# Kernel optimization log

Hardware: AMD Instinct MI355X
Metric: run time of the kernel (lower is better)

## Reference

```python
import jax, jax.numpy as jnp
import numpy as np

P = 8          # patch_size
HEADS = 4      # patch_size // 2
DIM = 256      # nf*P*P // 16
DH = DIM // HEADS


def setup_inputs() -> dict:
    key = jax.random.key(0)
    ks = jax.random.split(key, 8)
    B, N, C, H, W = 8, 1, 64, 256, 256
    Np = (H // P) * (W // P)           # 1024
    patch_dim = C * P * P              # 4096
    s = 0.02
    return {
        "x": jax.random.normal(ks[0], (B, N, C, H, W), jnp.float32),
        "W_embed": jax.random.normal(ks[1], (DIM, patch_dim), jnp.float32) * s,
        "b_embed": jnp.zeros((DIM,), jnp.float32),
        "pos": jax.random.normal(ks[2], (1, Np, DIM), jnp.float32),
        "Wq": jax.random.normal(ks[3], (DIM, DIM), jnp.float32) * s,
        "Wk": jax.random.normal(ks[4], (Np, Np), jnp.float32) * s,
        "Wv": jax.random.normal(ks[5], (DIM, DIM), jnp.float32) * s,
        "Wout": jax.random.normal(ks[6], (patch_dim, DIM), jnp.float32) * s,
        "b_out": jnp.zeros((patch_dim,), jnp.float32),
    }


def reference(x, W_embed, b_embed, pos, Wq, Wk, Wv, Wout, b_out):
    B, N, C, H, W = x.shape
    Hp, Wp = H // P, W // P
    Np = Hp * Wp
    patch_dim = C * P * P
    BN = B * N

    # unfold (non-overlapping patches), column order = (C, kh, kw)
    xb = x.reshape(BN, C, Hp, P, Wp, P)
    patches = xb.transpose(0, 2, 4, 1, 3, 5).reshape(BN, Np, patch_dim)

    # linear_embed + positional embedding
    emb = jnp.einsum('bnp,dp->bnd', patches, W_embed) + b_embed + pos  # (BN, Np, DIM)

    # q: linear, split heads, mean over head-dim (AvgPool1d(dh) on length dh)
    q = jnp.einsum('bnd,ed->bne', emb, Wq)
    q = q.reshape(BN, Np, HEADS, DH).transpose(0, 2, 1, 3)  # (BN, H, Np, DH)
    q = q.mean(axis=-1)                                      # (BN, H, Np)

    # k = sigmoid(linear_k(q)); diag_embed(k) @ v == k[..., None] * v
    k = jax.nn.sigmoid(jnp.einsum('bhn,mn->bhm', q, Wk))     # (BN, H, Np)

    v = jnp.einsum('bnd,ed->bne', emb, Wv)
    v = v.reshape(BN, Np, HEADS, DH).transpose(0, 2, 1, 3)   # (BN, H, Np, DH)

    out = k[..., None] * v                                   # (BN, H, Np, DH)
    out = out.transpose(0, 2, 1, 3).reshape(BN, Np, DIM)

    out = jnp.einsum('bnd,pd->bnp', out, Wout) + b_out       # (BN, Np, patch_dim)

    # fold back to image
    out = out.reshape(BN, Hp, Wp, C, P, P).transpose(0, 3, 1, 4, 2, 5)
    out = out.reshape(B, N, C, H, W)
    return out
```

## Files before the change

### kernel.cpp

```cpp
#include <hip/hip_runtime.h>

typedef __attribute__((ext_vector_type(8))) short short8;
typedef __attribute__((ext_vector_type(4))) float f32x4;

#define LDA 72
#define KST 260

__device__ __forceinline__ unsigned short f2bf(float f) {
  unsigned int u = __builtin_bit_cast(unsigned int, f);
  u += 0x7fffu + ((u >> 16) & 1u);
  return (unsigned short)(u >> 16);
}
__device__ __forceinline__ float bf2f(unsigned short us) {
  return __builtin_bit_cast(float, (unsigned int)us << 16);
}

__device__ __forceinline__ short8 cvt8(float4 lo, float4 hi) {
  short8 v;
  v[0] = (short)f2bf(lo.x); v[1] = (short)f2bf(lo.y);
  v[2] = (short)f2bf(lo.z); v[3] = (short)f2bf(lo.w);
  v[4] = (short)f2bf(hi.x); v[5] = (short)f2bf(hi.y);
  v[6] = (short)f2bf(hi.z); v[7] = (short)f2bf(hi.w);
  return v;
}

__device__ __forceinline__ void mfma_tile(const unsigned short* __restrict__ Ab,
                                          const unsigned short* __restrict__ Bb,
                                          int wm, int wn, int lr, int lq,
                                          f32x4 (&acc)[2][4]) {
#pragma unroll
  for (int kc = 0; kc < 2; ++kc) {
    short8 a0 = *(const short8*)&Ab[(wm * 32 + lr) * LDA + kc * 32 + lq * 8];
    short8 a1 = *(const short8*)&Ab[(wm * 32 + 16 + lr) * LDA + kc * 32 + lq * 8];
#pragma unroll
    for (int ni = 0; ni < 4; ++ni) {
      short8 b = *(const short8*)&Bb[(wn * 64 + ni * 16 + lr) * LDA + kc * 32 + lq * 8];
      acc[0][ni] = __builtin_amdgcn_mfma_f32_16x16x32_bf16(a0, b, acc[0][ni], 0, 0, 0);
      acc[1][ni] = __builtin_amdgcn_mfma_f32_16x16x32_bf16(a1, b, acc[1][ni], 0, 0, 0);
    }
  }
}

__device__ __forceinline__ void cvt_block(const float* __restrict__ src,
                                          unsigned short* __restrict__ dst, int b) {
  int i = b * 256 + threadIdx.x;
  float4 f = ((const float4*)src)[i];
  unsigned int lo = (unsigned int)f2bf(f.x) | ((unsigned int)f2bf(f.y) << 16);
  unsigned int hi = (unsigned int)f2bf(f.z) | ((unsigned int)f2bf(f.w) << 16);
  uint2 u; u.x = lo; u.y = hi;
  ((uint2*)dst)[i] = u;
}

__global__ __launch_bounds__(256) void prep_kernel(
    const float* __restrict__ W_embed, const float* __restrict__ Wout,
    const float* __restrict__ Wv, const float* __restrict__ Wq,
    unsigned short* __restrict__ Wb, unsigned short* __restrict__ Wob,
    unsigned short* __restrict__ Wvb, float* __restrict__ WqR) {
  int b = blockIdx.x;
  if (b < 1024) { cvt_block(W_embed, Wb, b); return; }
  if (b < 2048) { cvt_block(Wout, Wob, b - 1024); return; }
  if (b < 2112) { cvt_block(Wv, Wvb, b - 2048); return; }
  int idx = (b - 2112) * 256 + threadIdx.x;
  int h = idx >> 8, e = idx & 255;
  float s = 0.f;
  for (int j = 0; j < 64; ++j) s += Wq[(size_t)(h * 64 + j) * 256 + e];
  WqR[idx] = s * (1.f / 64.f);
}

struct StageG1 { float4 a0, a1, a2, a3; short8 b0, b1; };

__device__ __forceinline__ void g1_load(StageG1& s, const float* q0, const float* q1,
                                        const unsigned short* b0, const unsigned short* b1) {
  s.a0 = *(const float4*)q0; s.a1 = *(const float4*)(q0 + 4);
  s.a2 = *(const float4*)q1; s.a3 = *(const float4*)(q1 + 4);
  s.b0 = *(const short8*)b0; s.b1 = *(const short8*)b1;
}

__device__ __forceinline__ void g1_write(unsigned short* Aw, unsigned short* Bw,
                                         int dA0, int dA1, int dB0, int dB1,
                                         const StageG1& s) {
  *(short8*)&Aw[dA0] = cvt8(s.a0, s.a1);
  *(short8*)&Aw[dA1] = cvt8(s.a2, s.a3);
  *(short8*)&Bw[dB0] = s.b0;
  *(short8*)&Bw[dB1] = s.b1;
}

__global__ __launch_bounds__(512, 4) void gemm1_embed(
    const float* __restrict__ x, const unsigned short* __restrict__ Wb,
    float* __restrict__ part) {
  __shared__ __align__(16) unsigned short sm[2][2][128 * LDA];
  const int nt = blockIdx.x, mt = blockIdx.y, sk = blockIdx.z;
  const int m0 = mt * 128, n0 = nt * 128;
  const int t = threadIdx.x;
  const int wave = t >> 6, lane = t & 63;
  const int wm = wave >> 1, wn = wave & 1;
  const int lr = lane & 15, lq = lane >> 4;

  const int bn = m0 >> 10;
  const int ph0 = (m0 & 1023) >> 5;

  const int uA0 = t >> 5, colA = t & 31;
  const int uA1 = uA0 + 16;
  const float* xA = x + ((size_t)(bn << 6) << 16);
  const float* pa0 = xA + (size_t)(((ph0 + (uA0 >> 3)) << 3) + (uA0 & 7)) * 256 + (colA << 3);
  const float* pa1 = xA + (size_t)(((ph0 + (uA1 >> 3)) << 3) + (uA1 & 7)) * 256 + (colA << 3);
  const int dA0 = (((uA0 >> 3) << 5) + colA) * LDA + ((uA0 & 7) << 3);
  const int dA1 = (((uA1 >> 3) << 5) + colA) * LDA + ((uA1 & 7) << 3);

  const int nB0 = t >> 3, kB = t & 7;
  const int nB1 = nB0 + 64;
  const unsigned short* pb0 = Wb + (size_t)(n0 + nB0) * 4096 + (kB << 3);
  const unsigned short* pb1 = Wb + (size_t)(n0 + nB1) * 4096 + (kB << 3);
  const int dB0 = nB0 * LDA + (kB << 3);
  const int dB1 = nB1 * LDA + (kB << 3);

  f32x4 acc[2][4];
#pragma unroll
  for (int i = 0; i < 2; i++)
#pragma unroll
    for (int j = 0; j < 4; j++) acc[i][j] = f32x4{0.f, 0.f, 0.f, 0.f};

  unsigned short* A0 = &sm[0][0][0]; unsigned short* B0 = &sm[0][1][0];
  unsigned short* A1 = &sm[1][0][0]; unsigned short* B1 = &sm[1][1][0];

  StageG1 st0, st1;
  const int kt0 = sk * 16;
  g1_load(st0, pa0 + (size_t)kt0 * 65536, pa1 + (size_t)kt0 * 65536,
          pb0 + (size_t)kt0 * 64, pb1 + (size_t)kt0 * 64);
  g1_load(st1, pa0 + (size_t)(kt0 + 1) * 65536, pa1 + (size_t)(kt0 + 1) * 65536,
          pb0 + (size_t)(kt0 + 1) * 64, pb1 + (size_t)(kt0 + 1) * 64);
  g1_write(A0, B0, dA0, dA1, dB0, dB1, st0);
  __syncthreads();

#pragma unroll 1
  for (int p = 0; p < 7; ++p) {
    const int kb = kt0 + 2 * p;
    g1_load(st0, pa0 + (size_t)(kb + 2) * 65536, pa1 + (size_t)(kb + 2) * 65536,
            pb0 + (size_t)(kb + 2) * 64, pb1 + (size_t)(kb + 2) * 64);
    mfma_tile(A0, B0, wm, wn, lr, lq, acc);
    g1_write(A1, B1, dA0, dA1, dB0, dB1, st1);
    __syncthreads();
    g1_load(st1, pa0 + (size_t)(kb + 3) * 65536, pa1 + (size_t)(kb + 3) * 65536,
            pb0 + (size_t)(kb + 3) * 64, pb1 + (size_t)(kb + 3) * 64);
    mfma_tile(A1, B1, wm, wn, lr, lq, acc);
    g1_write(A0, B0, dA0, dA1, dB0, dB1, st0);
    __syncthreads();
  }
  mfma_tile(A0, B0, wm, wn, lr, lq, acc);
  g1_write(A1, B1, dA0, dA1, dB0, dB1, st1);
  __syncthreads();
  mfma_tile(A1, B1, wm, wn, lr, lq, acc);

  float* pdst = part + (size_t)sk * 2097152;
#pragma unroll
  for (int mi = 0; mi < 2; ++mi)
#pragma unroll
    for (int ni = 0; ni < 4; ++ni) {
      int col = n0 + wn * 64 + ni * 16 + lr;
      int rbase = m0 + wm * 32 + mi * 16 + lq * 4;
#pragma unroll
      for (int r2 = 0; r2 < 4; ++r2)
        pdst[(size_t)(rbase + r2) * 256 + col] = acc[mi][ni][r2];
    }
}

__global__ __launch_bounds__(256) void finq_kernel(
    const float* __restrict__ part, const float* __restrict__ b_embed,
    const float* __restrict__ pos, const float* __restrict__ WqR,
    unsigned short* __restrict__ emb_bf, float* __restrict__ q) {
  __shared__ float wq[1024];
  const int t = threadIdx.x;
  for (int i = t; i < 1024; i += 256) wq[i] = WqR[i];
  __syncthreads();
  const int row_l = t >> 3, seg = t & 7;
  const int row = blockIdx.x * 32 + row_l;
  const int bn = row >> 10, n = row & 1023;
  const float4* p4 = (const float4*)part;
  const float4* b4 = (const float4*)b_embed;
  const float4* pos4 = (const float4*)pos;
  const float4* wq4 = (const float4*)wq;
  const int idx0 = row * 64 + seg * 8;

  float4 e[8];
#pragma unroll
  for (int j = 0; j < 8; ++j) {
    float4 v = p4[idx0 + j];
    float4 v1 = p4[524288 + idx0 + j];
    float4 v2 = p4[1048576 + idx0 + j];
    float4 v3 = p4[1572864 + idx0 + j];
    float4 bb = b4[seg * 8 + j];
    float4 pp = pos4[(size_t)n * 64 + seg * 8 + j];
    e[j].x = v.x + v1.x + v2.x + v3.x + bb.x + pp.x;
    e[j].y = v.y + v1.y + v2.y + v3.y + bb.y + pp.y;
    e[j].z = v.z + v1.z + v2.z + v3.z + bb.z + pp.z;
    e[j].w = v.w + v1.w + v2.w + v3.w + bb.w + pp.w;
  }
  unsigned int ub[16];
#pragma unroll
  for (int j = 0; j < 8; ++j) {
    ub[2 * j]     = (unsigned int)f2bf(e[j].x) | ((unsigned int)f2bf(e[j].y) << 16);
    ub[2 * j + 1] = (unsigned int)f2bf(e[j].z) | ((unsigned int)f2bf(e[j].w) << 16);
  }
  uint4* dst = (uint4*)(emb_bf + (size_t)row * 256 + seg * 32);
#pragma unroll
  for (int j = 0; j < 4; ++j)
    dst[j] = make_uint4(ub[4 * j], ub[4 * j + 1], ub[4 * j + 2], ub[4 * j + 3]);
  float s[4] = {0.f, 0.f, 0.f, 0.f};
#pragma unroll
  for (int h = 0; h < 4; ++h)
#pragma unroll
    for (int j = 0; j < 8; ++j) {
      float4 w = wq4[h * 64 + seg * 8 + j];
      s[h] += e[j].x * w.x + e[j].y * w.y + e[j].z * w.z + e[j].w * w.w;
    }
#pragma unroll
  for (int h = 0; h < 4; ++h) {
    s[h] += __shfl_xor(s[h], 1);
    s[h] += __shfl_xor(s[h], 2);
    s[h] += __shfl_xor(s[h], 4);
  }
  if (seg == 0) {
#pragma unroll
    for (int h = 0; h < 4; ++h)
      q[(size_t)(bn * 4 + h) * 1024 + n] = s[h];
  }
}

__global__ __launch_bounds__(256) void k_kernel(const float* __restrict__ q,
                                                const float* __restrict__ Wk,
                                                float* __restrict__ kk) {
  __shared__ float wk_s[8 * KST];
  __shared__ float q_s[32 * KST];
  const int m0 = blockIdx.x * 8;
  const int t = threadIdx.x;
  const int m = t & 7, bh = t >> 3;
  const float4* wkg = (const float4*)Wk;
  const float4* qg = (const float4*)q;
  float acc = 0.f;
  for (int kt = 0; kt < 4; ++kt) {
    const int k0 = kt * 256;
#pragma unroll
    for (int i = 0; i < 2; ++i) {
      int idx = t + i * 256;
      int r = idx >> 6, c4 = idx & 63;
      *(float4*)&wk_s[r * KST + c4 * 4] = wkg[((size_t)(m0 + r) * 1024 + k0) / 4 + c4];
    }
#pragma unroll
    for (int i = 0; i < 8; ++i) {
      int idx = t + i * 256;
      int r = idx >> 6, c4 = idx & 63;
      *(float4*)&q_s[r * KST + c4 * 4] = qg[((size_t)r * 1024 + k0) / 4 + c4];
    }
    __syncthreads();
#pragma unroll 8
    for (int k4 = 0; k4 < 64; ++k4) {
      float4 a = *(const float4*)&wk_s[m * KST + k4 * 4];
      float4 b = *(const float4*)&q_s[bh * KST + k4 * 4];
      acc += a.x * b.x + a.y * b.y + a.z * b.z + a.w * b.w;
    }
    __syncthreads();
  }
  kk[(size_t)bh * 1024 + m0 + m] = 1.f / (1.f + __expf(-acc));
}

#define VST 264
__global__ __launch_bounds__(256) void vgemm_kernel(
    const unsigned short* __restrict__ Abf, const unsigned short* __restrict__ Wvb,
    const float* __restrict__ kk, unsigned short* __restrict__ ov) {
  __shared__ __align__(16) unsigned short Vs[128 * VST];
  const int nt = blockIdx.x, mt = blockIdx.y;
  const int m0 = mt * 64, n0 = nt * 64;
  const int t = threadIdx.x;
  const int wave = t >> 6, lane = t & 63;
  const int wr = wave >> 1, wc = wave & 1;
  const int lr = lane & 15, lq = lane >> 4;

  const int row0 = t >> 5, kb = t & 31;
#pragma unroll
  for (int i = 0; i < 8; ++i)
    *(short8*)&Vs[(row0 + i * 8) * VST + kb * 8] =
        *(const short8*)(Abf + (size_t)(m0 + row0 + i * 8) * 256 + kb * 8);
#pragma unroll
  for (int i = 0; i < 8; ++i)
    *(short8*)&Vs[(64 + row0 + i * 8) * VST + kb * 8] =
        *(const short8*)(Wvb + (size_t)(n0 + row0 + i * 8) * 256 + kb * 8);
  __syncthreads();

  f32x4 acc[2][2];
#pragma unroll
  for (int i = 0; i < 2; ++i)
#pragma unroll
    for (int j = 0; j < 2; ++j) acc[i][j] = f32x4{0.f, 0.f, 0.f, 0.f};

#pragma unroll
  for (int kc = 0; kc < 8; ++kc) {
    short8 a0 = *(const short8*)&Vs[(wr * 32 + lr) * VST + kc * 32 + lq * 8];
    short8 a1 = *(const short8*)&Vs[(wr * 32 + 16 + lr) * VST + kc * 32 + lq * 8];
    short8 b0 = *(const short8*)&Vs[(64 + wc * 32 + lr) * VST + kc * 32 + lq * 8];
    short8 b1 = *(const short8*)&Vs[(64 + wc * 32 + 16 + lr) * VST + kc * 32 + lq * 8];
    acc[0][0] = __builtin_amdgcn_mfma_f32_16x16x32_bf16(a0, b0, acc[0][0], 0, 0, 0);
    acc[0][1] = __builtin_amdgcn_mfma_f32_16x16x32_bf16(a0, b1, acc[0][1], 0, 0, 0);
    acc[1][0] = __builtin_amdgcn_mfma_f32_16x16x32_bf16(a1, b0, acc[1][0], 0, 0, 0);
    acc[1][1] = __builtin_amdgcn_mfma_f32_16x16x32_bf16(a1, b1, acc[1][1], 0, 0, 0);
  }

#pragma unroll
  for (int mi = 0; mi < 2; ++mi)
#pragma unroll
    for (int ni = 0; ni < 2; ++ni) {
      int col = n0 + wc * 32 + ni * 16 + lr;
      int h = col >> 6;
      int rbase = m0 + wr * 32 + mi * 16 + lq * 4;
#pragma unroll
      for (int r2 = 0; r2 < 4; ++r2) {
        int row = rbase + r2;
        int bn = row >> 10, n = row & 1023;
        float g = kk[(size_t)(bn * 4 + h) * 1024 + n];
        ov[(size_t)row * 256 + col] = f2bf(acc[mi][ni][r2] * g);
      }
    }
}

#define CST 132
struct StageG2 { short8 a[2]; short8 b[4]; };

__device__ __forceinline__ void g2_load(StageG2& s, const unsigned short* pA,
                                        const unsigned short* pB, int k0) {
#pragma unroll
  for (int i = 0; i < 2; ++i)
    s.a[i] = *(const short8*)(pA + (size_t)i * 32 * 256 + k0);
#pragma unroll
  for (int i = 0; i < 4; ++i)
    s.b[i] = *(const short8*)(pB + (size_t)i * 32 * 256 + k0);
}
__device__ __forceinline__ void g2_write(unsigned short* Ab, unsigned short* Bb,
                                         int dA, int dB, const StageG2& s) {
#pragma unroll
  for (int i = 0; i < 2; ++i) *(short8*)&Ab[dA + i * 32 * LDA] = s.a[i];
#pragma unroll
  for (int i = 0; i < 4; ++i) *(short8*)&Bb[dB + i * 32 * LDA] = s.b[i];
}

__global__ __launch_bounds__(256, 2) void gemm2_out(
    const unsigned short* __restrict__ Abf, const unsigned short* __restrict__ Wob,
    const float* __restrict__ b_out, float* __restrict__ out) {
  __shared__ __align__(16) unsigned short smbuf[2][192 * LDA];
  float* csm = (float*)&smbuf[0][0];
  const int nt = blockIdx.x, mt = blockIdx.y;
  const int m0 = mt * 64, n0 = nt * 128;
  const int t = threadIdx.x;
  const int wave = t >> 6, lane = t & 63;
  const int wm = wave >> 1, wn = wave & 1;
  const int lr = lane & 15, lq = lane >> 4;

  unsigned short* A0 = &smbuf[0][0]; unsigned short* B0 = &smbuf[0][64 * LDA];
  unsigned short* A1 = &smbuf[1][0]; unsigned short* B1 = &smbuf[1][64 * LDA];

  const unsigned short* pA = Abf + (size_t)(m0 + (t >> 3)) * 256 + (t & 7) * 8;
  const unsigned short* pB = Wob + (size_t)(n0 + (t >> 3)) * 256 + (t & 7) * 8;
  const int dA = (t >> 3) * LDA + (t & 7) * 8;
  const int dB = dA;

  f32x4 acc[2][4];
#pragma unroll
  for (int i = 0; i < 2; i++)
#pragma unroll
    for (int j = 0; j < 4; j++) acc[i][j] = f32x4{0.f, 0.f, 0.f, 0.f};

  StageG2 st0, st1;
  g2_load(st0, pA, pB, 0);
  g2_load(st1, pA, pB, 64);
  g2_write(A0, B0, dA, dB, st0);
  __syncthreads();
  g2_load(st0, pA, pB, 128);
  mfma_tile(A0, B0, wm, wn, lr, lq, acc);
  g2_write(A1, B1, dA, dB, st1);
  __syncthreads();
  g2_load(st1, pA, pB, 192);
  mfma_tile(A1, B1, wm, wn, lr, lq, acc);
  g2_write(A0, B0, dA, dB, st0);
  __syncthreads();
  mfma_tile(A0, B0, wm, wn, lr, lq, acc);
  g2_write(A1, B1, dA, dB, st1);
  __syncthreads();
  mfma_tile(A1, B1, wm, wn, lr, lq, acc);
  __syncthreads();

#pragma unroll
  for (int mi = 0; mi < 2; ++mi)
#pragma unroll
    for (int ni = 0; ni < 4; ++ni) {
      int pl = wn * 64 + ni * 16 + lr;
      int mb = wm * 32 + mi * 16 + lq * 4;
#pragma unroll
      for (int r2 = 0; r2 < 4; ++r2)
        csm[(mb + r2) * CST + pl] = acc[mi][ni][r2];
    }
  __syncthreads();
  const int bn = m0 >> 10;
  const int ph0 = (m0 & 1023) >> 5;
  const int c0 = n0 >> 6;
#pragma unroll
  for (int i = 0; i < 8; ++i) {
    int idx4 = t + i * 256;
    int kw4 = idx4 & 1;
    int pw = (idx4 >> 1) & 31;
    int kh = (idx4 >> 6) & 7;
    int c2 = (idx4 >> 9) & 1;
    int ph = (idx4 >> 10) & 1;
    int m_local = ph * 32 + pw;
    int p_local = c2 * 64 + kh * 8 + kw4 * 4;
    float4 v = *(const float4*)&csm[m_local * CST + p_local];
    float4 bo = *(const float4*)(b_out + n0 + p_local);
    v.x += bo.x; v.y += bo.y; v.z += bo.z; v.w += bo.w;
    size_t addr = ((size_t)((bn << 6) + c0 + c2) << 16) +
                  (size_t)(((ph0 + ph) << 3) + kh) * 256 + (pw << 3) + kw4 * 4;
    *(float4*)(out + addr) = v;
  }
}

extern "C" void kernel_launch(void* const* d_in, const int* in_sizes, int n_in,
                              void* d_out, int out_size, void* d_ws, size_t ws_size,
                              hipStream_t stream) {
  const float* x       = (const float*)d_in[0];
  const float* W_embed = (const float*)d_in[1];
  const float* b_embed = (const float*)d_in[2];
  const float* pos     = (const float*)d_in[3];
  const float* Wq      = (const float*)d_in[4];
  const float* Wk      = (const float*)d_in[5];
  const float* Wv      = (const float*)d_in[6];
  const float* Wout    = (const float*)d_in[7];
  const float* b_out   = (const float*)d_in[8];
  float* out = (float*)d_out;

  char* ws = (char*)d_ws;
  const size_t MB = 1024 * 1024;
  float* part            = (float*)(ws);
  unsigned short* ov     = (unsigned short*)(ws);
  unsigned short* emb_bf = (unsigned short*)(ws + 32 * MB);
  unsigned short* Wb     = (unsigned short*)(ws + 36 * MB);
  unsigned short* Wob    = (unsigned short*)(ws + 38 * MB);
  unsigned short* Wvb    = (unsigned short*)(ws + 40 * MB);
  float* q               = (float*)(ws + 40 * MB + 131072);
  float* kk              = (float*)(ws + 40 * MB + 262144);
  float* WqR             = (float*)(ws + 40 * MB + 393216);

  prep_kernel<<<2116, 256, 0, stream>>>(W_embed, Wout, Wv, Wq, Wb, Wob, Wvb, WqR);
  gemm1_embed<<<dim3(2, 64, 4), 512, 0, stream>>>(x, Wb, part);
  finq_kernel<<<256, 256, 0, stream>>>(part, b_embed, pos, WqR, emb_bf, q);
  k_kernel<<<128, 256, 0, stream>>>(q, Wk, kk);
  vgemm_kernel<<<dim3(4, 128), 256, 0, stream>>>(emb_bf, Wvb, kk, ov);
  gemm2_out<<<dim3(32, 128), 256, 0, stream>>>(ov, Wob, b_out, out);
}
```

Baseline: 334.0 us.

## Fuse embed GEMM with bias/pos/q epilogue, drop split-K partials

Replaces the split-K embed GEMM (128x128 tiles, 4 K-splits writing fp32 partials) and the separate finalize kernel with one kernel. Each block computes a 32x256 output tile over the full K and applies bias, positional embedding, bf16 conversion and the q projection from LDS. This removes the 32MB partial-sum round trip and one launch. In exchange the grid shrinks to 256 blocks of 256 threads with a long serial K loop, and each block rereads the full W_embed slice, which may lower parallelism and raise weight traffic.

```diff
diff --git a/kernel.cpp b/kernel.cpp
--- a/kernel.cpp
+++ b/kernel.cpp
@@ -67,52 +67,38 @@
   WqR[idx] = s * (1.f / 64.f);
 }
 
-struct StageG1 { float4 a0, a1, a2, a3; short8 b0, b1; };
-
-__device__ __forceinline__ void g1_load(StageG1& s, const float* q0, const float* q1,
-                                        const unsigned short* b0, const unsigned short* b1) {
-  s.a0 = *(const float4*)q0; s.a1 = *(const float4*)(q0 + 4);
-  s.a2 = *(const float4*)q1; s.a3 = *(const float4*)(q1 + 4);
-  s.b0 = *(const short8*)b0; s.b1 = *(const short8*)b1;
-}
-
-__device__ __forceinline__ void g1_write(unsigned short* Aw, unsigned short* Bw,
-                                         int dA0, int dA1, int dB0, int dB1,
-                                         const StageG1& s) {
-  *(short8*)&Aw[dA0] = cvt8(s.a0, s.a1);
-  *(short8*)&Aw[dA1] = cvt8(s.a2, s.a3);
-  *(short8*)&Bw[dB0] = s.b0;
-  *(short8*)&Bw[dB1] = s.b1;
-}
-
-__global__ __launch_bounds__(512, 4) void gemm1_embed(
+struct StageV3 { float4 a0, a1; short8 b[8]; };
+
+__global__ __launch_bounds__(256, 1) void gemm1_fused(
     const float* __restrict__ x, const unsigned short* __restrict__ Wb,
-    float* __restrict__ part) {
-  __shared__ __align__(16) unsigned short sm[2][2][128 * LDA];
-  const int nt = blockIdx.x, mt = blockIdx.y, sk = blockIdx.z;
-  const int m0 = mt * 128, n0 = nt * 128;
+    const float* __restrict__ b_embed, const float* __restrict__ pos,
+    const float* __restrict__ WqR,
+    unsigned short* __restrict__ emb_bf, float* __restrict__ q) {
+  __shared__ __align__(16) unsigned short lds[41472];
+  __shared__ float wq_s[1024];
+  unsigned short* A0 = lds;
+  unsigned short* A1 = lds + 2304;
+  unsigned short* B0 = lds + 4608;
+  unsigned short* B1 = lds + 23040;
+  float* esm = (float*)(lds + 4608);
+
   const int t = threadIdx.x;
   const int wave = t >> 6, lane = t & 63;
-  const int wm = wave >> 1, wn = wave & 1;
+  const int wn = wave;
   const int lr = lane & 15, lq = lane >> 4;
-
+  const int m0 = blockIdx.x * 32;
   const int bn = m0 >> 10;
-  const int ph0 = (m0 & 1023) >> 5;
-
-  const int uA0 = t >> 5, colA = t & 31;
-  const int uA1 = uA0 + 16;
-  const float* xA = x + ((size_t)(bn << 6) << 16);
-  const float* pa0 = xA + (size_t)(((ph0 + (uA0 >> 3)) << 3) + (uA0 & 7)) * 256 + (colA << 3);
-  const float* pa1 = xA + (size_t)(((ph0 + (uA1 >> 3)) << 3) + (uA1 & 7)) * 256 + (colA << 3);
-  const int dA0 = (((uA0 >> 3) << 5) + colA) * LDA + ((uA0 & 7) << 3);
-  const int dA1 = (((uA1 >> 3) << 5) + colA) * LDA + ((uA1 & 7) << 3);
-
-  const int nB0 = t >> 3, kB = t & 7;
-  const int nB1 = nB0 + 64;
-  const unsigned short* pb0 = Wb + (size_t)(n0 + nB0) * 4096 + (kB << 3);
-  const unsigned short* pb1 = Wb + (size_t)(n0 + nB1) * 4096 + (kB << 3);
-  const int dB0 = nB0 * LDA + (kB << 3);
-  const int dB1 = nB1 * LDA + (kB << 3);
+  const int nbase = m0 & 1023;
+  const int ph = nbase >> 5;
+
+  for (int i = t; i < 1024; i += 256) wq_s[i] = WqR[i];
+
+  const int mA = t >> 3, kc8 = t & 7;
+  const float* pa = x + ((size_t)(bn << 6) << 16) +
+                    (size_t)((ph << 3) + kc8) * 256 + (mA << 3);
+  const int dA = mA * LDA + (kc8 << 3);
+  const unsigned short* pb = Wb + (size_t)(t >> 3) * 4096 + ((t & 7) << 3);
+  const int dB = (t >> 3) * LDA + ((t & 7) << 3);
 
   f32x4 acc[2][4];
 #pragma unroll
@@ -120,110 +106,105 @@
 #pragma unroll
     for (int j = 0; j < 4; j++) acc[i][j] = f32x4{0.f, 0.f, 0.f, 0.f};
 
-  unsigned short* A0 = &sm[0][0][0]; unsigned short* B0 = &sm[0][1][0];
-  unsigned short* A1 = &sm[1][0][0]; unsigned short* B1 = &sm[1][1][0];
-
-  StageG1 st0, st1;
-  const int kt0 = sk * 16;
-  g1_load(st0, pa0 + (size_t)kt0 * 65536, pa1 + (size_t)kt0 * 65536,
-          pb0 + (size_t)kt0 * 64, pb1 + (size_t)kt0 * 64);
-  g1_load(st1, pa0 + (size_t)(kt0 + 1) * 65536, pa1 + (size_t)(kt0 + 1) * 65536,
-          pb0 + (size_t)(kt0 + 1) * 64, pb1 + (size_t)(kt0 + 1) * 64);
-  g1_write(A0, B0, dA0, dA1, dB0, dB1, st0);
+  StageV3 st0, st1;
+#define G1F_LOAD(st, kt)                                                         \
+  {                                                                              \
+    const float* qa = pa + (size_t)(kt) * 65536;                                 \
+    st.a0 = *(const float4*)qa; st.a1 = *(const float4*)(qa + 4);                \
+    _Pragma("unroll")                                                            \
+    for (int i = 0; i < 8; ++i)                                                  \
+      st.b[i] = *(const short8*)(pb + (size_t)i * 131072 + (kt) * 64);           \
+  }
+#define G1F_WRITE(st, Aw, Bw)                                                    \
+  {                                                                              \
+    *(short8*)&Aw[dA] = cvt8(st.a0, st.a1);                                      \
+    _Pragma("unroll")                                                            \
+    for (int i = 0; i < 8; ++i) *(short8*)&Bw[dB + i * 32 * LDA] = st.b[i];      \
+  }
+
+  G1F_LOAD(st0, 0)
+  G1F_LOAD(st1, 1)
+  G1F_WRITE(st0, A0, B0)
   __syncthreads();
 
 #pragma unroll 1
-  for (int p = 0; p < 7; ++p) {
-    const int kb = kt0 + 2 * p;
-    g1_load(st0, pa0 + (size_t)(kb + 2) * 65536, pa1 + (size_t)(kb + 2) * 65536,
-            pb0 + (size_t)(kb + 2) * 64, pb1 + (size_t)(kb + 2) * 64);
-    mfma_tile(A0, B0, wm, wn, lr, lq, acc);
-    g1_write(A1, B1, dA0, dA1, dB0, dB1, st1);
+  for (int p = 0; p < 31; ++p) {
+    G1F_LOAD(st0, 2 * p + 2)
+    mfma_tile(A0, B0, 0, wn, lr, lq, acc);
+    G1F_WRITE(st1, A1, B1)
     __syncthreads();
-    g1_load(st1, pa0 + (size_t)(kb + 3) * 65536, pa1 + (size_t)(kb + 3) * 65536,
-            pb0 + (size_t)(kb + 3) * 64, pb1 + (size_t)(kb + 3) * 64);
-    mfma_tile(A1, B1, wm, wn, lr, lq, acc);
-    g1_write(A0, B0, dA0, dA1, dB0, dB1, st0);
+    G1F_LOAD(st1, 2 * p + 3)
+    mfma_tile(A1, B1, 0, wn, lr, lq, acc);
+    G1F_WRITE(st0, A0, B0)
     __syncthreads();
   }
-  mfma_tile(A0, B0, wm, wn, lr, lq, acc);
-  g1_write(A1, B1, dA0, dA1, dB0, dB1, st1);
-  __syncthreads();
-  mfma_tile(A1, B1, wm, wn, lr, lq, acc);
-
-  float* pdst = part + (size_t)sk * 2097152;
+  mfma_tile(A0, B0, 0, wn, lr, lq, acc);
+  G1F_WRITE(st1, A1, B1)
+  __syncthreads();
+  mfma_tile(A1, B1, 0, wn, lr, lq, acc);
+
 #pragma unroll
   for (int mi = 0; mi < 2; ++mi)
 #pragma unroll
     for (int ni = 0; ni < 4; ++ni) {
-      int col = n0 + wn * 64 + ni * 16 + lr;
-      int rbase = m0 + wm * 32 + mi * 16 + lq * 4;
+      int col = wn * 64 + ni * 16 + lr;
+      int rb = mi * 16 + lq * 4;
 #pragma unroll
       for (int r2 = 0; r2 < 4; ++r2)
-        pdst[(size_t)(rbase + r2) * 256 + col] = acc[mi][ni][r2];
-    }
-}
-
-__global__ __launch_bounds__(256) void finq_kernel(
-    const float* __restrict__ part, const float* __restrict__ b_embed,
-    const float* __restrict__ pos, const float* __restrict__ WqR,
-    unsigned short* __restrict__ emb_bf, float* __restrict__ q) {
-  __shared__ float wq[1024];
-  const int t = threadIdx.x;
-  for (int i = t; i < 1024; i += 256) wq[i] = WqR[i];
-  __syncthreads();
-  const int row_l = t >> 3, seg = t & 7;
-  const int row = blockIdx.x * 32 + row_l;
-  const int bn = row >> 10, n = row & 1023;
-  const float4* p4 = (const float4*)part;
-  const float4* b4 = (const float4*)b_embed;
-  const float4* pos4 = (const float4*)pos;
-  const float4* wq4 = (const float4*)wq;
-  const int idx0 = row * 64 + seg * 8;
-
-  float4 e[8];
-#pragma unroll
-  for (int j = 0; j < 8; ++j) {
-    float4 v = p4[idx0 + j];
-    float4 v1 = p4[524288 + idx0 + j];
-    float4 v2 = p4[1048576 + idx0 + j];
-    float4 v3 = p4[1572864 + idx0 + j];
-    float4 bb = b4[seg * 8 + j];
-    float4 pp = pos4[(size_t)n * 64 + seg * 8 + j];
-    e[j].x = v.x + v1.x + v2.x + v3.x + bb.x + pp.x;
-    e[j].y = v.y + v1.y + v2.y + v3.y + bb.y + pp.y;
-    e[j].z = v.z + v1.z + v2.z + v3.z + bb.z + pp.z;
-    e[j].w = v.w + v1.w + v2.w + v3.w + bb.w + pp.w;
-  }
-  unsigned int ub[16];
-#pragma unroll
-  for (int j = 0; j < 8; ++j) {
-    ub[2 * j]     = (unsigned int)f2bf(e[j].x) | ((unsigned int)f2bf(e[j].y) << 16);
-    ub[2 * j + 1] = (unsigned int)f2bf(e[j].z) | ((unsigned int)f2bf(e[j].w) << 16);
-  }
-  uint4* dst = (uint4*)(emb_bf + (size_t)row * 256 + seg * 32);
-#pragma unroll
-  for (int j = 0; j < 4; ++j)
-    dst[j] = make_uint4(ub[4 * j], ub[4 * j + 1], ub[4 * j + 2], ub[4 * j + 3]);
-  float s[4] = {0.f, 0.f, 0.f, 0.f};
-#pragma unroll
-  for (int h = 0; h < 4; ++h)
+        esm[(rb + r2) * 264 + col] = acc[mi][ni][r2];
+    }
+  __syncthreads();
+
+  {
+    const int row = t >> 3, seg = t & 7;
+    const int n = nbase + row;
+    const float4* e4 = (const float4*)esm;
+    const float4* b4 = (const float4*)b_embed;
+    const float4* pos4 = (const float4*)pos;
+    const float4* wq4 = (const float4*)wq_s;
+    float4 e[8];
 #pragma unroll
     for (int j = 0; j < 8; ++j) {
-      float4 w = wq4[h * 64 + seg * 8 + j];
-      s[h] += e[j].x * w.x + e[j].y * w.y + e[j].z * w.z + e[j].w * w.w;
-    }
-#pragma unroll
-  for (int h = 0; h < 4; ++h) {
-    s[h] += __shfl_xor(s[h], 1);
-    s[h] += __shfl_xor(s[h], 2);
-    s[h] += __shfl_xor(s[h], 4);
-  }
-  if (seg == 0) {
+      float4 v = e4[row * 66 + seg * 8 + j];
+      float4 bb = b4[seg * 8 + j];
+      float4 pp = pos4[(size_t)n * 64 + seg * 8 + j];
+      e[j].x = v.x + bb.x + pp.x;
+      e[j].y = v.y + bb.y + pp.y;
+      e[j].z = v.z + bb.z + pp.z;
+      e[j].w = v.w + bb.w + pp.w;
+    }
+    unsigned int ub[16];
+#pragma unroll
+    for (int j = 0; j < 8; ++j) {
+      ub[2 * j]     = (unsigned int)f2bf(e[j].x) | ((unsigned int)f2bf(e[j].y) << 16);
+      ub[2 * j + 1] = (unsigned int)f2bf(e[j].z) | ((unsigned int)f2bf(e[j].w) << 16);
+    }
+    uint4* dst = (uint4*)(emb_bf + (size_t)(m0 + row) * 256 + seg * 32);
+#pragma unroll
+    for (int j = 0; j < 4; ++j)
+      dst[j] = make_uint4(ub[4 * j], ub[4 * j + 1], ub[4 * j + 2], ub[4 * j + 3]);
+    float s[4] = {0.f, 0.f, 0.f, 0.f};
 #pragma unroll
     for (int h = 0; h < 4; ++h)
-      q[(size_t)(bn * 4 + h) * 1024 + n] = s[h];
-  }
+#pragma unroll
+      for (int j = 0; j < 8; ++j) {
+        float4 w = wq4[h * 64 + seg * 8 + j];
+        s[h] += e[j].x * w.x + e[j].y * w.y + e[j].z * w.z + e[j].w * w.w;
+      }
+#pragma unroll
+    for (int h = 0; h < 4; ++h) {
+      s[h] += __shfl_xor(s[h], 1);
+      s[h] += __shfl_xor(s[h], 2);
+      s[h] += __shfl_xor(s[h], 4);
+    }
+    if (seg == 0) {
+#pragma unroll
+      for (int h = 0; h < 4; ++h)
+        q[(size_t)(bn * 4 + h) * 1024 + n] = s[h];
+    }
+  }
+#undef G1F_LOAD
+#undef G1F_WRITE
 }
 
 __global__ __launch_bounds__(256) void k_kernel(const float* __restrict__ q,
@@ -435,19 +416,17 @@
 
   char* ws = (char*)d_ws;
   const size_t MB = 1024 * 1024;
-  float* part            = (float*)(ws);
-  unsigned short* ov     = (unsigned short*)(ws);
-  unsigned short* emb_bf = (unsigned short*)(ws + 32 * MB);
-  unsigned short* Wb     = (unsigned short*)(ws + 36 * MB);
-  unsigned short* Wob    = (unsigned short*)(ws + 38 * MB);
-  unsigned short* Wvb    = (unsigned short*)(ws + 40 * MB);
-  float* q               = (float*)(ws + 40 * MB + 131072);
-  float* kk              = (float*)(ws + 40 * MB + 262144);
-  float* WqR             = (float*)(ws + 40 * MB + 393216);
+  unsigned short* emb_bf = (unsigned short*)(ws);
+  unsigned short* ov     = (unsigned short*)(ws + 4 * MB);
+  unsigned short* Wb     = (unsigned short*)(ws + 8 * MB);
+  unsigned short* Wob    = (unsigned short*)(ws + 10 * MB);
+  unsigned short* Wvb    = (unsigned short*)(ws + 12 * MB);
+  float* q               = (float*)(ws + 12 * MB + 131072);
+  float* kk              = (float*)(ws + 12 * MB + 262144);
+  float* WqR             = (float*)(ws + 12 * MB + 393216);
 
   prep_kernel<<<2116, 256, 0, stream>>>(W_embed, Wout, Wv, Wq, Wb, Wob, Wvb, WqR);
-  gemm1_embed<<<dim3(2, 64, 4), 512, 0, stream>>>(x, Wb, part);
-  finq_kernel<<<256, 256, 0, stream>>>(part, b_embed, pos, WqR, emb_bf, q);
+  gemm1_fused<<<256, 256, 0, stream>>>(x, Wb, b_embed, pos, WqR, emb_bf, q);
   k_kernel<<<128, 256, 0, stream>>>(q, Wk, kk);
   vgemm_kernel<<<dim3(4, 128), 256, 0, stream>>>(emb_bf, Wvb, kk, ov);
   gemm2_out<<<dim3(32, 128), 256, 0, stream>>>(ov, Wob, b_out, out);
```

New measurement: 323.2 us. 3.2% less time.
